# Kernel optimization log

Measured on AMD Instinct MI355X. Metric: run time of the kernel, lower is better.

The kernel has to match this reference:

```python
import jax, jax.numpy as jnp
import numpy as np

NUM_HEADS = 16
NEG = -1000000.0


def setup_inputs() -> dict:
    key = jax.random.key(0)
    ks = jax.random.split(key, 10)
    B, S, H = 2, 2048, 2048
    inp = {
        "X": jax.random.normal(ks[0], (B, S, H), dtype=jnp.float32),
        "attention_mask": jax.random.randint(ks[1], (B, S), 0, 2, dtype=jnp.int32),
    }
    names = ["W_q", "W_k", "W_v", "W_q_m", "W_k_m", "W_v_m", "W_o"]
    for i, n in enumerate(names):
        # matches torch.randn(H, H) / 100 init scale
        inp[n] = jax.random.normal(ks[2 + i], (H, H), dtype=jnp.float32) / 100.0
    return inp


def reference(X, attention_mask, W_q, W_k, W_v, W_q_m, W_k_m, W_v_m, W_o):
    B, S, H = X.shape
    nh, hd = NUM_HEADS, H // NUM_HEADS

    Q = X @ W_q
    K = X @ W_k
    V = X @ W_v
    Q_m = Q @ W_q_m
    K_m = K @ W_k_m
    V_m = V @ W_v_m

    # Faithful to the original: reshape (B, S, H) -> (B, nh, S, H/nh)
    # (row-major reshape, i.e. a sequence-chunked 'head' split, NOT a
    # standard feature-dim head split).
    Qs = Q_m.reshape(B, nh, S, hd)
    Ks = K_m.reshape(B, nh, S, hd)
    Vs = V_m.reshape(B, nh, S, hd)

    # scores: (B, nh, S, S)
    scores = jnp.einsum("bhqd,bhkd->bhqk", Qs, Ks)

    m1 = attention_mask[:, None, :, None]  # (B,1,S,1)
    m2 = attention_mask[:, None, None, :]  # (B,1,1,S)
    scores = jnp.where(m1 == 0, NEG, scores)
    scores = jnp.where(m2 == 0, NEG, scores)

    weights = jax.nn.softmax(scores, axis=-1)
    out = jnp.einsum("bhqk,bhkd->bhqd", weights, Vs)  # (B, nh, S, hd)
    out = out.reshape(B, S, H)  # faithful inverse reshape
    return out @ W_o
```

## Files before the change

### kernel.cpp

```cpp
#include <hip/hip_runtime.h>
#include <hip/hip_bf16.h>

typedef __bf16 bf16x8 __attribute__((ext_vector_type(8)));
typedef float f32x4 __attribute__((ext_vector_type(4)));
typedef unsigned short u16;

__device__ __forceinline__ u16 f2bf(float f) {
  __bf16 b = (__bf16)f;
  return __builtin_bit_cast(u16, b);
}
__device__ __forceinline__ float bf2f(u16 v) {
  unsigned int u = ((unsigned int)v) << 16;
  return __builtin_bit_cast(float, u);
}

struct PrepArgs {
  const float* X; u16* Xb;
  const float* Wsrc[3]; u16* Wdst[3];
  const float* Tsrc[3]; u16* Tdst[3];
};

__global__ void prep(PrepArgs a) {
  __shared__ float t[32][33];
  const int blk = blockIdx.x, tid = threadIdx.x;
  if (blk < 8192) {
    int i = blk * 256 + tid;
    float4 f = reinterpret_cast<const float4*>(a.X)[i];
    ushort4 o;
    o.x = f2bf(f.x); o.y = f2bf(f.y); o.z = f2bf(f.z); o.w = f2bf(f.w);
    reinterpret_cast<ushort4*>(a.Xb)[i] = o;
  } else if (blk < 20480) {
    int r = blk - 8192;
    int z = r >> 12;
    int i = (r & 4095) * 256 + tid;
    float4 f = reinterpret_cast<const float4*>(a.Wsrc[z])[i];
    ushort4 o;
    o.x = f2bf(f.x); o.y = f2bf(f.y); o.z = f2bf(f.z); o.w = f2bf(f.w);
    reinterpret_cast<ushort4*>(a.Wdst[z])[i] = o;
  } else {
    int r = blk - 20480;
    int z = r >> 12;
    int rem = r & 4095;
    int bx = rem & 63, by = rem >> 6;
    const float* src = a.Tsrc[z];
    u16* dst = a.Tdst[z];
    int tx = tid & 31, ty = tid >> 5;
#pragma unroll
    for (int i = 0; i < 4; ++i)
      t[ty + i * 8][tx] = src[(size_t)(by * 32 + ty + i * 8) * 2048 + bx * 32 + tx];
    __syncthreads();
#pragma unroll
    for (int i = 0; i < 4; ++i)
      dst[(size_t)(bx * 32 + ty + i * 8) * 2048 + by * 32 + tx] = f2bf(t[tx][ty + i * 8]);
  }
}

__global__ void post_transpose(const u16* __restrict__ Vm, u16* __restrict__ VT,
                               const float* __restrict__ Wo, u16* __restrict__ WoT) {
  __shared__ u16 ts[32][33];
  __shared__ float tf[32][33];
  const int blk = blockIdx.x, tid = threadIdx.x;
  const int tx = tid & 31, ty = tid >> 5;
  if (blk < 8192) {
    int slab = blk >> 8;
    int rem = blk & 255;
    int bx = rem & 63, by = rem >> 6;
    const u16* s = Vm + (size_t)slab * 2048 * 128;
    u16* d = VT + (size_t)slab * 128 * 2048;
#pragma unroll
    for (int i = 0; i < 4; ++i)
      ts[ty + i * 8][tx] = s[(size_t)(bx * 32 + ty + i * 8) * 128 + by * 32 + tx];
    __syncthreads();
#pragma unroll
    for (int i = 0; i < 4; ++i)
      d[(size_t)(by * 32 + ty + i * 8) * 2048 + bx * 32 + tx] = ts[tx][ty + i * 8];
  } else {
    int rem = blk - 8192;
    int bx = rem & 63, by = rem >> 6;
#pragma unroll
    for (int i = 0; i < 4; ++i)
      tf[ty + i * 8][tx] = Wo[(size_t)(by * 32 + ty + i * 8) * 2048 + bx * 32 + tx];
    __syncthreads();
#pragma unroll
    for (int i = 0; i < 4; ++i)
      WoT[(size_t)(bx * 32 + ty + i * 8) * 2048 + by * 32 + tx] = f2bf(tf[tx][ty + i * 8]);
  }
}

struct GemmArgs { const u16* A[3]; const u16* B[3]; void* C[3]; };

#define SBARF() do { __builtin_amdgcn_sched_barrier(0); __builtin_amdgcn_s_barrier(); \
                     __builtin_amdgcn_sched_barrier(0); } while (0)
#define LGKM0() do { asm volatile("s_waitcnt lgkmcnt(0)" ::: "memory"); \
                     __builtin_amdgcn_sched_barrier(0); } while (0)
#define VMC4()  do { asm volatile("s_waitcnt vmcnt(4)" ::: "memory"); \
                     __builtin_amdgcn_sched_barrier(0); } while (0)
#define VMC0()  do { asm volatile("s_waitcnt vmcnt(0)" ::: "memory"); \
                     __builtin_amdgcn_sched_barrier(0); } while (0)

__device__ __forceinline__ void gll16(const u16* gp, u16* lp) {
  __builtin_amdgcn_global_load_lds((const __attribute__((address_space(1))) void*)gp,
                                   (__attribute__((address_space(3))) void*)lp, 16, 0, 0);
}

template <bool F32OUT>
__global__ __launch_bounds__(512, 2)
void gemm8(GemmArgs g, int M, int N, int K) {
  (void)M;
  extern __shared__ u16 lds[];
  const u16* A = g.A[blockIdx.z];
  const u16* B = g.B[blockIdx.z];
  const int tid = threadIdx.x;
  const int lane = tid & 63, w = tid >> 6;
  const int wm = w >> 2, wn = w & 3;
  const int l15 = lane & 15, quad = lane >> 4;
  const int m0 = blockIdx.y * 256, n0 = blockIdx.x * 256;

  const int srow = tid & 127;
  const int sks8 = (tid >> 7) * 8;
  const int swu = w * 512;

  auto stage = [&](int buf, int mat, int half, int kt) {
    const u16* src = mat ? B : A;
    const size_t g0 = (size_t)((mat ? n0 : m0) + half * 128 + srow) * K
                    + (size_t)kt * 64 + sks8;
    u16* l0 = lds + buf * 32768 + (mat * 2 + half) * 8192 + swu;
    gll16(src + g0, l0);
    gll16(src + g0 + 32, l0 + 4096);
  };

  const int aoff = wm * 8192 + quad * 1024 + l15 * 8;
  const int boff = 16384 + (wn >> 1) * 8192 + quad * 1024 + ((wn & 1) * 64 + l15) * 8;

  const f32x4 zf = {0.f, 0.f, 0.f, 0.f};
  f32x4 acc[8][4];
#pragma unroll
  for (int i = 0; i < 8; ++i)
#pragma unroll
    for (int j = 0; j < 4; ++j) acc[i][j] = zf;

  bf16x8 aP[2][2], aR[6][2], bF[4][2];

#define LDB_ALL(buf_) do { _Pragma("unroll") for (int nt = 0; nt < 4; ++nt) { \
    const u16* p_ = lds + (buf_) * 32768 + boff + nt * 128; \
    bF[nt][0] = *reinterpret_cast<const bf16x8*>(p_); \
    bF[nt][1] = *reinterpret_cast<const bf16x8*>(p_ + 4096); } } while (0)
#define LDA2(buf_) do { _Pragma("unroll") for (int mi = 0; mi < 2; ++mi) { \
    const u16* p_ = lds + (buf_) * 32768 + aoff + mi * 128; \
    aP[mi][0] = *reinterpret_cast<const bf16x8*>(p_); \
    aP[mi][1] = *reinterpret_cast<const bf16x8*>(p_ + 4096); } } while (0)
#define LDA6(buf_) do { _Pragma("unroll") for (int mi = 0; mi < 6; ++mi) { \
    const u16* p_ = lds + (buf_) * 32768 + aoff + (mi + 2) * 128; \
    aR[mi][0] = *reinterpret_cast<const bf16x8*>(p_); \
    aR[mi][1] = *reinterpret_cast<const bf16x8*>(p_ + 4096); } } while (0)

#define MQUAD(A0_, A1_, M0_, M1_) do { \
    __builtin_amdgcn_s_setprio(1); \
    _Pragma("unroll") for (int s_ = 0; s_ < 2; ++s_) \
      _Pragma("unroll") for (int nt = 0; nt < 4; ++nt) { \
        acc[M0_][nt] = __builtin_amdgcn_mfma_f32_16x16x32_bf16(A0_[s_], bF[nt][s_], acc[M0_][nt], 0, 0, 0); \
        acc[M1_][nt] = __builtin_amdgcn_mfma_f32_16x16x32_bf16(A1_[s_], bF[nt][s_], acc[M1_][nt], 0, 0, 0); } \
    __builtin_amdgcn_s_setprio(0); \
    __builtin_amdgcn_sched_barrier(0); \
  } while (0)

  const int NT = K >> 6;
  const int NI = NT >> 1;

  stage(0, 0, 0, 0); stage(0, 0, 1, 0); stage(0, 1, 0, 0); stage(0, 1, 1, 0);
  stage(1, 0, 0, 1); stage(1, 0, 1, 1);
  VMC4();
  SBARF();

  for (int i = 0; i < NI; ++i) {
    const int te = 2 * i, to = te + 1;
    const bool pf = (i + 1 < NI);
    LDB_ALL(0); LDA2(0);
    stage(1, 1, 0, to);
    SBARF(); LGKM0();
    MQUAD(aP[0], aP[1], 0, 1);
    SBARF();
    LDA6(0);
    stage(1, 1, 1, to);
    SBARF(); LGKM0();
    MQUAD(aR[0], aR[1], 2, 3);
    SBARF();
    if (pf) stage(0, 0, 0, te + 2);
    SBARF();
    MQUAD(aR[2], aR[3], 4, 5);
    SBARF();
    if (pf) stage(0, 0, 1, te + 2);
    SBARF();
    MQUAD(aR[4], aR[5], 6, 7);
    if (pf) { VMC4(); } else { VMC0(); }
    SBARF();
    LDB_ALL(1); LDA2(1);
    if (pf) stage(0, 1, 0, te + 2);
    SBARF(); LGKM0();
    MQUAD(aP[0], aP[1], 0, 1);
    SBARF();
    LDA6(1);
    if (pf) stage(0, 1, 1, te + 2);
    SBARF(); LGKM0();
    MQUAD(aR[0], aR[1], 2, 3);
    SBARF();
    if (pf) stage(1, 0, 0, to + 2);
    SBARF();
    MQUAD(aR[2], aR[3], 4, 5);
    SBARF();
    if (pf) stage(1, 0, 1, to + 2);
    SBARF();
    MQUAD(aR[4], aR[5], 6, 7);
    VMC4();
    SBARF();
  }

#pragma unroll
  for (int mt = 0; mt < 8; ++mt)
#pragma unroll
    for (int nt = 0; nt < 4; ++nt)
#pragma unroll
      for (int r = 0; r < 4; ++r) {
        int mrow = m0 + wm * 128 + mt * 16 + quad * 4 + r;
        int ncol = n0 + wn * 64 + nt * 16 + l15;
        if constexpr (F32OUT)
          ((float*)g.C[blockIdx.z])[(size_t)mrow * N + ncol] = acc[mt][nt][r];
        else
          ((u16*)g.C[blockIdx.z])[(size_t)mrow * N + ncol] = f2bf(acc[mt][nt][r]);
      }
#undef LDB_ALL
#undef LDA2
#undef LDA6
#undef MQUAD
}

__global__ __launch_bounds__(256, 2)
void flash_attn(const u16* __restrict__ Qm, const u16* __restrict__ Km,
                const u16* __restrict__ VTr, const int* __restrict__ mask,
                u16* __restrict__ Out) {
  __shared__ __align__(16) u16 Ks[16 * 64 * 8];
  __shared__ __align__(16) u16 Vs[8 * 128 * 8];
  __shared__ __align__(16) u16 PL[4][32 * 64];
  __shared__ u16 Mf[2048];

  const int b = blockIdx.z, head = blockIdx.y, qb = blockIdx.x;
  const int slab = b * 16 + head;
  const u16* Qs = Qm + (size_t)slab * 2048 * 128;
  const u16* Kg = Km + (size_t)slab * 2048 * 128;
  const u16* Vg = VTr + (size_t)slab * 128 * 2048;
  u16* Og = Out + (size_t)slab * 2048 * 128;
  const int* mb = mask + b * 2048;

  const int tid = threadIdx.x;
  const int lane = tid & 63, w = tid >> 6;
  const int l15 = lane & 15, quad = lane >> 4;
  const int q0w = qb * 128 + w * 32;

#pragma unroll
  for (int j = 0; j < 8; ++j) {
    int i = j * 256 + tid;
    Mf[i] = mb[i] ? (u16)0x3F80 : (u16)0;
  }

  bf16x8 aQ[2][4];
#pragma unroll
  for (int mt = 0; mt < 2; ++mt)
#pragma unroll
    for (int c = 0; c < 4; ++c)
      aQ[mt][c] = *reinterpret_cast<const bf16x8*>(
          Qs + (size_t)(q0w + mt * 16 + l15) * 128 + c * 32 + quad * 8);

  int mq[2][4];
#pragma unroll
  for (int mt = 0; mt < 2; ++mt)
#pragma unroll
    for (int r = 0; r < 4; ++r) mq[mt][r] = mb[q0w + mt * 16 + quad * 4 + r];

  const f32x4 zf = {0.f, 0.f, 0.f, 0.f};
  float l_part[2][4];
  f32x4 acc[2][8];
#pragma unroll
  for (int mt = 0; mt < 2; ++mt) {
#pragma unroll
    for (int r = 0; r < 4; ++r) l_part[mt][r] = 0.f;
#pragma unroll
    for (int nd = 0; nd < 8; ++nd) acc[mt][nd] = zf;
  }

  __syncthreads();

  u16* PLw = PL[w];

  for (int k0 = 0; k0 < 2048; k0 += 64) {
#pragma unroll
    for (int t = 0; t < 8; ++t) {
      int idx = w * 8 + t;
      if (idx < 16) {
        const u16* gp = Kg + (size_t)(k0 + lane) * 128 + idx * 8;
        u16* lp = Ks + idx * 64 * 8;
        __builtin_amdgcn_global_load_lds((const __attribute__((address_space(1))) void*)gp,
                                         (__attribute__((address_space(3))) void*)lp,
                                         16, 0, 0);
      } else {
        int u = idx - 16, kc = u >> 1, dh = u & 1;
        const u16* gp = Vg + (size_t)(dh * 64 + lane) * 2048 + k0 + kc * 8;
        u16* lp = Vs + (kc * 128 + dh * 64) * 8;
        __builtin_amdgcn_global_load_lds((const __attribute__((address_space(1))) void*)gp,
                                         (__attribute__((address_space(3))) void*)lp,
                                         16, 0, 0);
      }
    }
    __syncthreads();

    f32x4 st[2][4];
#pragma unroll
    for (int mt = 0; mt < 2; ++mt)
#pragma unroll
      for (int nt = 0; nt < 4; ++nt) st[mt][nt] = zf;
#pragma unroll
    for (int c = 0; c < 4; ++c)
#pragma unroll
      for (int nt = 0; nt < 4; ++nt) {
        bf16x8 bK = *reinterpret_cast<const bf16x8*>(
            &Ks[((c * 4 + quad) * 64 + nt * 16 + l15) * 8]);
        st[0][nt] = __builtin_amdgcn_mfma_f32_16x16x32_bf16(aQ[0][c], bK, st[0][nt], 0, 0, 0);
        st[1][nt] = __builtin_amdgcn_mfma_f32_16x16x32_bf16(aQ[1][c], bK, st[1][nt], 0, 0, 0);
      }

    float mkf[4];
#pragma unroll
    for (int nt = 0; nt < 4; ++nt) mkf[nt] = bf2f(Mf[k0 + nt * 16 + l15]);

#pragma unroll
    for (int mt = 0; mt < 2; ++mt)
#pragma unroll
      for (int nt = 0; nt < 4; ++nt)
#pragma unroll
        for (int r = 0; r < 4; ++r) {
          float e = __expf(st[mt][nt][r]) * mkf[nt];
          float p = mq[mt][r] ? e : 1.0f;
          l_part[mt][r] += p;
          int row = mt * 16 + quad * 4 + r;
          int col = nt * 16 + l15;
          int addr = row * 64 + (((col >> 3) ^ (row & 7)) << 3) + (col & 7);
          PLw[addr] = f2bf(p);
        }

#pragma unroll
    for (int pc = 0; pc < 2; ++pc) {
      bf16x8 aP0 = *reinterpret_cast<const bf16x8*>(
          &PLw[(0 + l15) * 64 + (((pc * 4 + quad) ^ (l15 & 7)) << 3)]);
      bf16x8 aP1 = *reinterpret_cast<const bf16x8*>(
          &PLw[(16 + l15) * 64 + (((pc * 4 + quad) ^ (l15 & 7)) << 3)]);
#pragma unroll
      for (int nd = 0; nd < 8; ++nd) {
        bf16x8 bV = *reinterpret_cast<const bf16x8*>(
            &Vs[((pc * 4 + quad) * 128 + nd * 16 + l15) * 8]);
        acc[0][nd] = __builtin_amdgcn_mfma_f32_16x16x32_bf16(aP0, bV, acc[0][nd], 0, 0, 0);
        acc[1][nd] = __builtin_amdgcn_mfma_f32_16x16x32_bf16(aP1, bV, acc[1][nd], 0, 0, 0);
      }
    }
    __syncthreads();
  }

  float inv[2][4];
#pragma unroll
  for (int mt = 0; mt < 2; ++mt)
#pragma unroll
    for (int r = 0; r < 4; ++r) {
      float l = l_part[mt][r];
      l += __shfl_xor(l, 1, 16);
      l += __shfl_xor(l, 2, 16);
      l += __shfl_xor(l, 4, 16);
      l += __shfl_xor(l, 8, 16);
      inv[mt][r] = 1.0f / l;
    }
#pragma unroll
  for (int mt = 0; mt < 2; ++mt)
#pragma unroll
    for (int nd = 0; nd < 8; ++nd)
#pragma unroll
      for (int r = 0; r < 4; ++r)
        Og[(size_t)(q0w + mt * 16 + quad * 4 + r) * 128 + nd * 16 + l15] =
            f2bf(acc[mt][nd][r] * inv[mt][r]);
}

extern "C" void kernel_launch(void* const* d_in, const int* in_sizes, int n_in,
                              void* d_out, int out_size, void* d_ws, size_t ws_size,
                              hipStream_t stream) {
  const float* X    = (const float*)d_in[0];
  const int*   mask = (const int*)d_in[1];
  const float* W_q  = (const float*)d_in[2];
  const float* W_k  = (const float*)d_in[3];
  const float* W_v  = (const float*)d_in[4];
  const float* W_qm = (const float*)d_in[5];
  const float* W_km = (const float*)d_in[6];
  const float* W_vm = (const float*)d_in[7];
  const float* W_o  = (const float*)d_in[8];
  float* out = (float*)d_out;

  char* ws = (char*)d_ws;
  const size_t MB = 1ull << 20;
  u16* Xb    = (u16*)(ws);
  u16* Wc0   = (u16*)(ws + 16 * MB);
  u16* Wc1   = (u16*)(ws + 24 * MB);
  u16* Wc2   = (u16*)(ws + 32 * MB);
  u16* WmT0  = (u16*)(ws + 40 * MB);
  u16* WmT1  = (u16*)(ws + 48 * MB);
  u16* WmT2  = (u16*)(ws + 56 * MB);
  u16* WqqT0 = (u16*)(ws + 64 * MB);
  u16* WqqT1 = (u16*)(ws + 72 * MB);
  u16* WqqT2 = (u16*)(ws + 80 * MB);
  u16* Qm    = (u16*)(ws + 88 * MB);
  u16* Km    = (u16*)(ws + 104 * MB);
  u16* Vm    = (u16*)(ws + 120 * MB);
  u16* VT    = Wc0;
  u16* AO    = WmT0;
  u16* WoT   = WqqT0;

  static bool attr_done = false;
  if (!attr_done) {
    (void)hipFuncSetAttribute(reinterpret_cast<const void*>(&gemm8<false>),
                              hipFuncAttributeMaxDynamicSharedMemorySize, 131072);
    (void)hipFuncSetAttribute(reinterpret_cast<const void*>(&gemm8<true>),
                              hipFuncAttributeMaxDynamicSharedMemorySize, 131072);
    attr_done = true;
  }

  {
    PrepArgs a;
    a.X = X; a.Xb = Xb;
    a.Wsrc[0] = W_q;  a.Wsrc[1] = W_k;  a.Wsrc[2] = W_v;
    a.Wdst[0] = Wc0;  a.Wdst[1] = Wc1;  a.Wdst[2] = Wc2;
    a.Tsrc[0] = W_qm; a.Tsrc[1] = W_km; a.Tsrc[2] = W_vm;
    a.Tdst[0] = WmT0; a.Tdst[1] = WmT1; a.Tdst[2] = WmT2;
    prep<<<dim3(32768), dim3(256), 0, stream>>>(a);
  }

  {
    GemmArgs g{{WmT0, WmT1, WmT2}, {Wc0, Wc1, Wc2}, {WqqT0, WqqT1, WqqT2}};
    gemm8<false><<<dim3(8, 8, 3), dim3(512), 131072, stream>>>(g, 2048, 2048, 2048);
  }

  {
    GemmArgs g{{Xb, Xb, Xb}, {WqqT0, WqqT1, WqqT2}, {Qm, Km, Vm}};
    gemm8<false><<<dim3(8, 16, 3), dim3(512), 131072, stream>>>(g, 4096, 2048, 2048);
  }

  post_transpose<<<dim3(12288), dim3(256), 0, stream>>>(Vm, VT, W_o, WoT);

  flash_attn<<<dim3(16, 16, 2), dim3(256), 0, stream>>>(Qm, Km, VT, mask, AO);

  {
    GemmArgs g{{AO, AO, AO}, {WoT, WoT, WoT}, {out, out, out}};
    gemm8<true><<<dim3(8, 16, 1), dim3(512), 131072, stream>>>(g, 4096, 2048, 2048);
  }
}
```

Before: 574.6 us.

## Add 128x256-tile triple-buffered GEMM for X-projection and output GEMMs

Introduces a new GEMM kernel with 128x256 output tiles, per-tile 64-wide K stages and a three-buffer LDS ring (prefetch two tiles ahead). It replaces the 256x256 double-buffered kernel for the fused QKV projection and the W_o projection. The smaller tile doubles the block count, which should fill the CUs better, and the deeper pipeline hides more global latency. In exchange, each block reuses less data per load and needs more LDS (144KB), which may limit occupancy to one block per CU.

```diff
diff --git a/kernel.cpp b/kernel.cpp
--- a/kernel.cpp
+++ b/kernel.cpp
@@ -95,6 +95,8 @@
                      __builtin_amdgcn_sched_barrier(0); } while (0)
 #define VMC4()  do { asm volatile("s_waitcnt vmcnt(4)" ::: "memory"); \
                      __builtin_amdgcn_sched_barrier(0); } while (0)
+#define VMC6()  do { asm volatile("s_waitcnt vmcnt(6)" ::: "memory"); \
+                     __builtin_amdgcn_sched_barrier(0); } while (0)
 #define VMC0()  do { asm volatile("s_waitcnt vmcnt(0)" ::: "memory"); \
                      __builtin_amdgcn_sched_barrier(0); } while (0)
 
@@ -102,6 +104,16 @@
   __builtin_amdgcn_global_load_lds((const __attribute__((address_space(1))) void*)gp,
                                    (__attribute__((address_space(3))) void*)lp, 16, 0, 0);
 }
+
+#define MQUAD(A0_, A1_, M0_, M1_) do { \
+    __builtin_amdgcn_s_setprio(1); \
+    _Pragma("unroll") for (int s_ = 0; s_ < 2; ++s_) \
+      _Pragma("unroll") for (int nt = 0; nt < 4; ++nt) { \
+        acc[M0_][nt] = __builtin_amdgcn_mfma_f32_16x16x32_bf16(A0_[s_], bF[nt][s_], acc[M0_][nt], 0, 0, 0); \
+        acc[M1_][nt] = __builtin_amdgcn_mfma_f32_16x16x32_bf16(A1_[s_], bF[nt][s_], acc[M1_][nt], 0, 0, 0); } \
+    __builtin_amdgcn_s_setprio(0); \
+    __builtin_amdgcn_sched_barrier(0); \
+  } while (0)
 
 template <bool F32OUT>
 __global__ __launch_bounds__(512, 2)
@@ -141,28 +153,18 @@
 
   bf16x8 aP[2][2], aR[6][2], bF[4][2];
 
-#define LDB_ALL(buf_) do { _Pragma("unroll") for (int nt = 0; nt < 4; ++nt) { \
+#define LDB_ALL8(buf_) do { _Pragma("unroll") for (int nt = 0; nt < 4; ++nt) { \
     const u16* p_ = lds + (buf_) * 32768 + boff + nt * 128; \
     bF[nt][0] = *reinterpret_cast<const bf16x8*>(p_); \
     bF[nt][1] = *reinterpret_cast<const bf16x8*>(p_ + 4096); } } while (0)
-#define LDA2(buf_) do { _Pragma("unroll") for (int mi = 0; mi < 2; ++mi) { \
+#define LDA2_8(buf_) do { _Pragma("unroll") for (int mi = 0; mi < 2; ++mi) { \
     const u16* p_ = lds + (buf_) * 32768 + aoff + mi * 128; \
     aP[mi][0] = *reinterpret_cast<const bf16x8*>(p_); \
     aP[mi][1] = *reinterpret_cast<const bf16x8*>(p_ + 4096); } } while (0)
-#define LDA6(buf_) do { _Pragma("unroll") for (int mi = 0; mi < 6; ++mi) { \
+#define LDA6_8(buf_) do { _Pragma("unroll") for (int mi = 0; mi < 6; ++mi) { \
     const u16* p_ = lds + (buf_) * 32768 + aoff + (mi + 2) * 128; \
     aR[mi][0] = *reinterpret_cast<const bf16x8*>(p_); \
     aR[mi][1] = *reinterpret_cast<const bf16x8*>(p_ + 4096); } } while (0)
-
-#define MQUAD(A0_, A1_, M0_, M1_) do { \
-    __builtin_amdgcn_s_setprio(1); \
-    _Pragma("unroll") for (int s_ = 0; s_ < 2; ++s_) \
-      _Pragma("unroll") for (int nt = 0; nt < 4; ++nt) { \
-        acc[M0_][nt] = __builtin_amdgcn_mfma_f32_16x16x32_bf16(A0_[s_], bF[nt][s_], acc[M0_][nt], 0, 0, 0); \
-        acc[M1_][nt] = __builtin_amdgcn_mfma_f32_16x16x32_bf16(A1_[s_], bF[nt][s_], acc[M1_][nt], 0, 0, 0); } \
-    __builtin_amdgcn_s_setprio(0); \
-    __builtin_amdgcn_sched_barrier(0); \
-  } while (0)
 
   const int NT = K >> 6;
   const int NI = NT >> 1;
@@ -175,12 +177,12 @@
   for (int i = 0; i < NI; ++i) {
     const int te = 2 * i, to = te + 1;
     const bool pf = (i + 1 < NI);
-    LDB_ALL(0); LDA2(0);
+    LDB_ALL8(0); LDA2_8(0);
     stage(1, 1, 0, to);
     SBARF(); LGKM0();
     MQUAD(aP[0], aP[1], 0, 1);
     SBARF();
-    LDA6(0);
+    LDA6_8(0);
     stage(1, 1, 1, to);
     SBARF(); LGKM0();
     MQUAD(aR[0], aR[1], 2, 3);
@@ -194,12 +196,12 @@
     MQUAD(aR[4], aR[5], 6, 7);
     if (pf) { VMC4(); } else { VMC0(); }
     SBARF();
-    LDB_ALL(1); LDA2(1);
+    LDB_ALL8(1); LDA2_8(1);
     if (pf) stage(0, 1, 0, te + 2);
     SBARF(); LGKM0();
     MQUAD(aP[0], aP[1], 0, 1);
     SBARF();
-    LDA6(1);
+    LDA6_8(1);
     if (pf) stage(0, 1, 1, te + 2);
     SBARF(); LGKM0();
     MQUAD(aR[0], aR[1], 2, 3);
@@ -228,10 +230,109 @@
         else
           ((u16*)g.C[blockIdx.z])[(size_t)mrow * N + ncol] = f2bf(acc[mt][nt][r]);
       }
-#undef LDB_ALL
-#undef LDA2
-#undef LDA6
-#undef MQUAD
+#undef LDB_ALL8
+#undef LDA2_8
+#undef LDA6_8
+}
+
+template <bool F32OUT>
+__global__ __launch_bounds__(512, 2)
+void gemm128(GemmArgs g, int M, int N, int K) {
+  (void)M;
+  extern __shared__ u16 lds[];
+  const u16* A = g.A[blockIdx.z];
+  const u16* B = g.B[blockIdx.z];
+  const int tid = threadIdx.x;
+  const int lane = tid & 63, w = tid >> 6;
+  const int wm = w >> 2, wn = w & 3;
+  const int l15 = lane & 15, quad = lane >> 4;
+  const int m0 = blockIdx.y * 128, n0 = blockIdx.x * 256;
+
+  const int arow = tid & 127, aks = tid >> 7;
+  const int brow = tid & 255, bks = tid >> 8;
+  const int swu = w * 512;
+
+  auto stageA = [&](int bufo, int kt, int j) {
+    const u16* gp = A + (size_t)(m0 + arow) * K + (size_t)kt * 64 + (aks + j * 4) * 8;
+    gll16(gp, lds + bufo + j * 4096 + swu);
+  };
+  auto stageB = [&](int bufo, int kt, int j) {
+    const u16* gp = B + (size_t)(n0 + brow) * K + (size_t)kt * 64 + (bks + j * 2) * 8;
+    gll16(gp, lds + bufo + 8192 + j * 4096 + swu);
+  };
+
+  const int aoff = quad * 1024 + wm * 512 + l15 * 8;
+  const int boff = 8192 + quad * 2048 + wn * 512 + l15 * 8;
+
+  const f32x4 zf = {0.f, 0.f, 0.f, 0.f};
+  f32x4 acc[4][4];
+#pragma unroll
+  for (int i = 0; i < 4; ++i)
+#pragma unroll
+    for (int j = 0; j < 4; ++j) acc[i][j] = zf;
+
+  bf16x8 aP[2][2], aR[2][2], bF[4][2];
+
+#define LDB_ALLT(bo_) do { _Pragma("unroll") for (int nt = 0; nt < 4; ++nt) { \
+    const u16* p_ = lds + (bo_) + boff + nt * 128; \
+    bF[nt][0] = *reinterpret_cast<const bf16x8*>(p_); \
+    bF[nt][1] = *reinterpret_cast<const bf16x8*>(p_ + 8192); } } while (0)
+#define LDA01T(bo_) do { _Pragma("unroll") for (int mi = 0; mi < 2; ++mi) { \
+    const u16* p_ = lds + (bo_) + aoff + mi * 128; \
+    aP[mi][0] = *reinterpret_cast<const bf16x8*>(p_); \
+    aP[mi][1] = *reinterpret_cast<const bf16x8*>(p_ + 4096); } } while (0)
+#define LDA23T(bo_) do { _Pragma("unroll") for (int mi = 0; mi < 2; ++mi) { \
+    const u16* p_ = lds + (bo_) + aoff + (mi + 2) * 128; \
+    aR[mi][0] = *reinterpret_cast<const bf16x8*>(p_); \
+    aR[mi][1] = *reinterpret_cast<const bf16x8*>(p_ + 4096); } } while (0)
+
+  const int NT = K >> 6;
+
+#pragma unroll
+  for (int j = 0; j < 4; ++j) stageB(0, 0, j);
+#pragma unroll
+  for (int j = 0; j < 2; ++j) stageA(0, 0, j);
+#pragma unroll
+  for (int j = 0; j < 4; ++j) stageB(24576, 1, j);
+#pragma unroll
+  for (int j = 0; j < 2; ++j) stageA(24576, 1, j);
+  VMC6();
+  SBARF();
+
+  int bo = 0, bo2 = 49152;
+  for (int t = 0; t < NT; ++t) {
+    const bool pf = (t + 2 < NT);
+    LDB_ALLT(bo); LDA01T(bo);
+    if (pf) { stageB(bo2, t + 2, 0); stageB(bo2, t + 2, 1); stageA(bo2, t + 2, 0); }
+    SBARF(); LGKM0();
+    MQUAD(aP[0], aP[1], 0, 1);
+    SBARF();
+    LDA23T(bo);
+    if (pf) { stageB(bo2, t + 2, 2); stageB(bo2, t + 2, 3); stageA(bo2, t + 2, 1); }
+    SBARF(); LGKM0();
+    MQUAD(aR[0], aR[1], 2, 3);
+    if (pf) { VMC6(); } else { VMC0(); }
+    SBARF();
+    bo = (bo == 49152) ? 0 : bo + 24576;
+    bo2 = (bo2 == 49152) ? 0 : bo2 + 24576;
+  }
+
+#pragma unroll
+  for (int mt = 0; mt < 4; ++mt)
+#pragma unroll
+    for (int nt = 0; nt < 4; ++nt)
+#pragma unroll
+      for (int r = 0; r < 4; ++r) {
+        int mrow = m0 + wm * 64 + mt * 16 + quad * 4 + r;
+        int ncol = n0 + wn * 64 + nt * 16 + l15;
+        if constexpr (F32OUT)
+          ((float*)g.C[blockIdx.z])[(size_t)mrow * N + ncol] = acc[mt][nt][r];
+        else
+          ((u16*)g.C[blockIdx.z])[(size_t)mrow * N + ncol] = f2bf(acc[mt][nt][r]);
+      }
+#undef LDB_ALLT
+#undef LDA01T
+#undef LDA23T
 }
 
 __global__ __launch_bounds__(256, 2)
@@ -424,6 +525,10 @@
                               hipFuncAttributeMaxDynamicSharedMemorySize, 131072);
     (void)hipFuncSetAttribute(reinterpret_cast<const void*>(&gemm8<true>),
                               hipFuncAttributeMaxDynamicSharedMemorySize, 131072);
+    (void)hipFuncSetAttribute(reinterpret_cast<const void*>(&gemm128<false>),
+                              hipFuncAttributeMaxDynamicSharedMemorySize, 147456);
+    (void)hipFuncSetAttribute(reinterpret_cast<const void*>(&gemm128<true>),
+                              hipFuncAttributeMaxDynamicSharedMemorySize, 147456);
     attr_done = true;
   }
 
@@ -444,7 +549,7 @@
 
   {
     GemmArgs g{{Xb, Xb, Xb}, {WqqT0, WqqT1, WqqT2}, {Qm, Km, Vm}};
-    gemm8<false><<<dim3(8, 16, 3), dim3(512), 131072, stream>>>(g, 4096, 2048, 2048);
+    gemm128<false><<<dim3(8, 32, 3), dim3(512), 147456, stream>>>(g, 4096, 2048, 2048);
   }
 
   post_transpose<<<dim3(12288), dim3(256), 0, stream>>>(Vm, VT, W_o, WoT);
@@ -453,6 +558,6 @@
 
   {
     GemmArgs g{{AO, AO, AO}, {WoT, WoT, WoT}, {out, out, out}};
-    gemm8<true><<<dim3(8, 16, 1), dim3(512), 131072, stream>>>(g, 4096, 2048, 2048);
-  }
-}
+    gemm128<true><<<dim3(8, 32, 1), dim3(512), 147456, stream>>>(g, 4096, 2048, 2048);
+  }
+}
```

Measured after the change: 658.5 us. 1.15x slower.

## Double-buffer K/V tiles in flash attention with 512-thread blocks

Applied to the files above, without the earlier changes.

Flash attention now uses dynamic LDS with two K/V buffers, so the next 64-key tile loads asynchronously while the current tile is computed. Block size grows to 8 waves covering 256 query rows, halving grid size and sharing each K/V tile across more waves. The per-iteration barrier becomes a vmcnt wait plus a single barrier. The larger LDS footprint (100KB) and bigger blocks may reduce occupancy. The GEMM macros are renamed and moved only.

```diff
diff --git a/kernel.cpp b/kernel.cpp
--- a/kernel.cpp
+++ b/kernel.cpp
@@ -103,6 +103,16 @@
                                    (__attribute__((address_space(3))) void*)lp, 16, 0, 0);
 }
 
+#define MQUAD(A0_, A1_, M0_, M1_) do { \
+    __builtin_amdgcn_s_setprio(1); \
+    _Pragma("unroll") for (int s_ = 0; s_ < 2; ++s_) \
+      _Pragma("unroll") for (int nt = 0; nt < 4; ++nt) { \
+        acc[M0_][nt] = __builtin_amdgcn_mfma_f32_16x16x32_bf16(A0_[s_], bF[nt][s_], acc[M0_][nt], 0, 0, 0); \
+        acc[M1_][nt] = __builtin_amdgcn_mfma_f32_16x16x32_bf16(A1_[s_], bF[nt][s_], acc[M1_][nt], 0, 0, 0); } \
+    __builtin_amdgcn_s_setprio(0); \
+    __builtin_amdgcn_sched_barrier(0); \
+  } while (0)
+
 template <bool F32OUT>
 __global__ __launch_bounds__(512, 2)
 void gemm8(GemmArgs g, int M, int N, int K) {
@@ -141,28 +151,18 @@
 
   bf16x8 aP[2][2], aR[6][2], bF[4][2];
 
-#define LDB_ALL(buf_) do { _Pragma("unroll") for (int nt = 0; nt < 4; ++nt) { \
+#define LDB_ALL8(buf_) do { _Pragma("unroll") for (int nt = 0; nt < 4; ++nt) { \
     const u16* p_ = lds + (buf_) * 32768 + boff + nt * 128; \
     bF[nt][0] = *reinterpret_cast<const bf16x8*>(p_); \
     bF[nt][1] = *reinterpret_cast<const bf16x8*>(p_ + 4096); } } while (0)
-#define LDA2(buf_) do { _Pragma("unroll") for (int mi = 0; mi < 2; ++mi) { \
+#define LDA2_8(buf_) do { _Pragma("unroll") for (int mi = 0; mi < 2; ++mi) { \
     const u16* p_ = lds + (buf_) * 32768 + aoff + mi * 128; \
     aP[mi][0] = *reinterpret_cast<const bf16x8*>(p_); \
     aP[mi][1] = *reinterpret_cast<const bf16x8*>(p_ + 4096); } } while (0)
-#define LDA6(buf_) do { _Pragma("unroll") for (int mi = 0; mi < 6; ++mi) { \
+#define LDA6_8(buf_) do { _Pragma("unroll") for (int mi = 0; mi < 6; ++mi) { \
     const u16* p_ = lds + (buf_) * 32768 + aoff + (mi + 2) * 128; \
     aR[mi][0] = *reinterpret_cast<const bf16x8*>(p_); \
     aR[mi][1] = *reinterpret_cast<const bf16x8*>(p_ + 4096); } } while (0)
-
-#define MQUAD(A0_, A1_, M0_, M1_) do { \
-    __builtin_amdgcn_s_setprio(1); \
-    _Pragma("unroll") for (int s_ = 0; s_ < 2; ++s_) \
-      _Pragma("unroll") for (int nt = 0; nt < 4; ++nt) { \
-        acc[M0_][nt] = __builtin_amdgcn_mfma_f32_16x16x32_bf16(A0_[s_], bF[nt][s_], acc[M0_][nt], 0, 0, 0); \
-        acc[M1_][nt] = __builtin_amdgcn_mfma_f32_16x16x32_bf16(A1_[s_], bF[nt][s_], acc[M1_][nt], 0, 0, 0); } \
-    __builtin_amdgcn_s_setprio(0); \
-    __builtin_amdgcn_sched_barrier(0); \
-  } while (0)
 
   const int NT = K >> 6;
   const int NI = NT >> 1;
@@ -175,12 +175,12 @@
   for (int i = 0; i < NI; ++i) {
     const int te = 2 * i, to = te + 1;
     const bool pf = (i + 1 < NI);
-    LDB_ALL(0); LDA2(0);
+    LDB_ALL8(0); LDA2_8(0);
     stage(1, 1, 0, to);
     SBARF(); LGKM0();
     MQUAD(aP[0], aP[1], 0, 1);
     SBARF();
-    LDA6(0);
+    LDA6_8(0);
     stage(1, 1, 1, to);
     SBARF(); LGKM0();
     MQUAD(aR[0], aR[1], 2, 3);
@@ -194,12 +194,12 @@
     MQUAD(aR[4], aR[5], 6, 7);
     if (pf) { VMC4(); } else { VMC0(); }
     SBARF();
-    LDB_ALL(1); LDA2(1);
+    LDB_ALL8(1); LDA2_8(1);
     if (pf) stage(0, 1, 0, te + 2);
     SBARF(); LGKM0();
     MQUAD(aP[0], aP[1], 0, 1);
     SBARF();
-    LDA6(1);
+    LDA6_8(1);
     if (pf) stage(0, 1, 1, te + 2);
     SBARF(); LGKM0();
     MQUAD(aR[0], aR[1], 2, 3);
@@ -228,21 +228,16 @@
         else
           ((u16*)g.C[blockIdx.z])[(size_t)mrow * N + ncol] = f2bf(acc[mt][nt][r]);
       }
-#undef LDB_ALL
-#undef LDA2
-#undef LDA6
-#undef MQUAD
-}
-
-__global__ __launch_bounds__(256, 2)
+#undef LDB_ALL8
+#undef LDA2_8
+#undef LDA6_8
+}
+
+__global__ __launch_bounds__(512, 2)
 void flash_attn(const u16* __restrict__ Qm, const u16* __restrict__ Km,
                 const u16* __restrict__ VTr, const int* __restrict__ mask,
                 u16* __restrict__ Out) {
-  __shared__ __align__(16) u16 Ks[16 * 64 * 8];
-  __shared__ __align__(16) u16 Vs[8 * 128 * 8];
-  __shared__ __align__(16) u16 PL[4][32 * 64];
-  __shared__ u16 Mf[2048];
-
+  extern __shared__ u16 lds[];
   const int b = blockIdx.z, head = blockIdx.y, qb = blockIdx.x;
   const int slab = b * 16 + head;
   const u16* Qs = Qm + (size_t)slab * 2048 * 128;
@@ -254,11 +249,14 @@
   const int tid = threadIdx.x;
   const int lane = tid & 63, w = tid >> 6;
   const int l15 = lane & 15, quad = lane >> 4;
-  const int q0w = qb * 128 + w * 32;
-
-#pragma unroll
-  for (int j = 0; j < 8; ++j) {
-    int i = j * 256 + tid;
+  const int q0w = qb * 256 + w * 32;
+
+  u16* Mf = lds + 49152;
+  u16* PLw = lds + 32768 + w * 2048;
+
+#pragma unroll
+  for (int j = 0; j < 4; ++j) {
+    int i = j * 512 + tid;
     Mf[i] = mb[i] ? (u16)0x3F80 : (u16)0;
   }
 
@@ -276,6 +274,21 @@
 #pragma unroll
     for (int r = 0; r < 4; ++r) mq[mt][r] = mb[q0w + mt * 16 + quad * 4 + r];
 
+  auto stageKV = [&](int buf, int k0) {
+#pragma unroll
+    for (int t = 0; t < 4; ++t) {
+      int idx = w * 4 + t;
+      if (idx < 16) {
+        const u16* gp = Kg + (size_t)(k0 + lane) * 128 + idx * 8;
+        gll16(gp, lds + buf * 8192 + idx * 512);
+      } else {
+        int u = idx - 16, kc = u >> 1, dh = u & 1;
+        const u16* gp = Vg + (size_t)(dh * 64 + lane) * 2048 + k0 + kc * 8;
+        gll16(gp, lds + 16384 + buf * 8192 + (kc * 128 + dh * 64) * 8);
+      }
+    }
+  };
+
   const f32x4 zf = {0.f, 0.f, 0.f, 0.f};
   float l_part[2][4];
   f32x4 acc[2][8];
@@ -287,30 +300,16 @@
     for (int nd = 0; nd < 8; ++nd) acc[mt][nd] = zf;
   }
 
+  stageKV(0, 0);
   __syncthreads();
 
-  u16* PLw = PL[w];
-
-  for (int k0 = 0; k0 < 2048; k0 += 64) {
-#pragma unroll
-    for (int t = 0; t < 8; ++t) {
-      int idx = w * 8 + t;
-      if (idx < 16) {
-        const u16* gp = Kg + (size_t)(k0 + lane) * 128 + idx * 8;
-        u16* lp = Ks + idx * 64 * 8;
-        __builtin_amdgcn_global_load_lds((const __attribute__((address_space(1))) void*)gp,
-                                         (__attribute__((address_space(3))) void*)lp,
-                                         16, 0, 0);
-      } else {
-        int u = idx - 16, kc = u >> 1, dh = u & 1;
-        const u16* gp = Vg + (size_t)(dh * 64 + lane) * 2048 + k0 + kc * 8;
-        u16* lp = Vs + (kc * 128 + dh * 64) * 8;
-        __builtin_amdgcn_global_load_lds((const __attribute__((address_space(1))) void*)gp,
-                                         (__attribute__((address_space(3))) void*)lp,
-                                         16, 0, 0);
-      }
-    }
-    __syncthreads();
+  for (int t = 0; t < 32; ++t) {
+    const int cur = t & 1;
+    const int k0 = t * 64;
+    if (t + 1 < 32) stageKV(cur ^ 1, k0 + 64);
+
+    const u16* Ks = lds + cur * 8192;
+    const u16* Vs = lds + 16384 + cur * 8192;
 
     f32x4 st[2][4];
 #pragma unroll
@@ -360,7 +359,9 @@
         acc[1][nd] = __builtin_amdgcn_mfma_f32_16x16x32_bf16(aP1, bV, acc[1][nd], 0, 0, 0);
       }
     }
-    __syncthreads();
+
+    VMC0();
+    SBARF();
   }
 
   float inv[2][4];
@@ -424,6 +425,8 @@
                               hipFuncAttributeMaxDynamicSharedMemorySize, 131072);
     (void)hipFuncSetAttribute(reinterpret_cast<const void*>(&gemm8<true>),
                               hipFuncAttributeMaxDynamicSharedMemorySize, 131072);
+    (void)hipFuncSetAttribute(reinterpret_cast<const void*>(&flash_attn),
+                              hipFuncAttributeMaxDynamicSharedMemorySize, 102400);
     attr_done = true;
   }
 
@@ -449,7 +452,7 @@
 
   post_transpose<<<dim3(12288), dim3(256), 0, stream>>>(Vm, VT, W_o, WoT);
 
-  flash_attn<<<dim3(16, 16, 2), dim3(256), 0, stream>>>(Qm, Km, VT, mask, AO);
+  flash_attn<<<dim3(8, 16, 2), dim3(512), 102400, stream>>>(Qm, Km, VT, mask, AO);
 
   {
     GemmArgs g{{AO, AO, AO}, {WoT, WoT, WoT}, {out, out, out}};
```

Result: faster. 551.0 us (-4.1%).
